# Kernel tuning notes

Hardware: AMD Instinct MI355X
Metric: run time of the kernel (lower is better)

The kernel has to match this reference:

```python
import jax, jax.numpy as jnp
from jax import lax
import numpy as np

B, C, N, T, K = 16, 64, 512, 64, 2
KSIZE, DIL = 2, 1
PAD = (KSIZE - 1) * DIL
EPS = 1e-5


def _powers(A, k):
    Ps = [jnp.eye(A.shape[0], dtype=A.dtype)]
    for _ in range(k):
        Ps.append(Ps[-1] @ A)
    return jnp.stack(Ps)  # (K+1, N, N)


def setup_inputs() -> dict:
    key = jax.random.key(0)
    ks = jax.random.split(key, 12)
    x = jax.random.normal(ks[0], (B, C, N, T), dtype=jnp.float32)
    # row-normalized random transition matrices, precomputed powers
    Af = jax.random.uniform(ks[1], (N, N), dtype=jnp.float32)
    Af = Af / Af.sum(axis=1, keepdims=True)
    Ab = Af.T / Af.T.sum(axis=1, keepdims=True)
    Aa = jax.random.uniform(ks[2], (N, N), dtype=jnp.float32)
    Aa = Aa / Aa.sum(axis=1, keepdims=True)
    P_f_pows = _powers(Af, K)
    P_b_pows = _powers(Ab, K)
    A_adp_pows = _powers(Aa, K)
    s = 0.05
    filter_w = jax.random.normal(ks[3], (C, C, 1, KSIZE), dtype=jnp.float32) * s
    filter_b = jnp.zeros((C,), jnp.float32)
    gate_w = jax.random.normal(ks[4], (C, C, 1, KSIZE), dtype=jnp.float32) * s
    gate_b = jnp.zeros((C,), jnp.float32)
    skip_w = jax.random.normal(ks[5], (C, C, 1, 1), dtype=jnp.float32) * s
    skip_b = jnp.zeros((C,), jnp.float32)
    weight_f = jax.random.normal(ks[6], (K + 1, C, C), dtype=jnp.float32) * s
    weight_b = jax.random.normal(ks[7], (K + 1, C, C), dtype=jnp.float32) * s
    gcn_bias = jnp.zeros((C,), jnp.float32)
    ln_gamma = jnp.ones((C,), jnp.float32)
    ln_beta = jnp.zeros((C,), jnp.float32)
    alpha = jnp.float32(0.5)
    return dict(x=x, P_f_pows=P_f_pows, P_b_pows=P_b_pows, A_adp_pows=A_adp_pows,
                filter_w=filter_w, filter_b=filter_b, gate_w=gate_w, gate_b=gate_b,
                skip_w=skip_w, skip_b=skip_b, weight_f=weight_f, weight_b=weight_b,
                gcn_bias=gcn_bias, ln_gamma=ln_gamma, ln_beta=ln_beta, alpha=alpha)


def _conv(x, w, b, dil=1):
    y = lax.conv_general_dilated(x, w, window_strides=(1, 1), padding='VALID',
                                 rhs_dilation=(1, dil),
                                 dimension_numbers=('NCHW', 'OIHW', 'NCHW'))
    return y + b[None, :, None, None]


def _apply_powers(xt, P_pows, weights):
    # xt: (B*T, N, Cin); P_pows: (K+1, N, N); weights: (K+1, Cin, Cout)
    xk = jnp.einsum('kij,bjc->kbic', P_pows, xt)
    return jnp.einsum('kbic,kco->bio', xk, weights)


def reference(x, P_f_pows, P_b_pows, A_adp_pows,
              filter_w, filter_b, gate_w, gate_b, skip_w, skip_b,
              weight_f, weight_b, gcn_bias, ln_gamma, ln_beta, alpha):
    # --- Gated TCN (causal left-pad along time) ---
    x_pad = jnp.pad(x, ((0, 0), (0, 0), (0, 0), (PAD, 0)))
    f = jnp.tanh(_conv(x_pad, filter_w, filter_b, DIL))
    g = jax.nn.sigmoid(_conv(x_pad, gate_w, gate_b, DIL))
    out = f * g                                   # (B, C, N, T)
    skip = _conv(out, skip_w, skip_b)             # 1x1 conv
    x_temporal = x + out                          # in_channels == out_channels

    # --- Diffusion GCN on (B*T, N, C) ---
    xt = jnp.transpose(x_temporal, (0, 3, 2, 1)).reshape(B * T, N, C)
    static_out = (_apply_powers(xt, P_f_pows, weight_f)
                  + _apply_powers(xt, P_b_pows, weight_b)
                  + gcn_bias[None, None, :])
    adapt_out = (_apply_powers(xt, A_adp_pows, weight_f)
                 + _apply_powers(xt, A_adp_pows, weight_b)
                 + gcn_bias[None, None, :])

    a = jax.nn.sigmoid(alpha)
    x_gcn = a * static_out + (1.0 - a) * adapt_out

    # --- LayerNorm over channel dim (dropout = identity in eval) ---
    mu = x_gcn.mean(axis=-1, keepdims=True)
    var = ((x_gcn - mu) ** 2).mean(axis=-1, keepdims=True)
    x_gcn = (x_gcn - mu) * lax.rsqrt(var + EPS) * ln_gamma + ln_beta

    x_out = x_gcn.reshape(B, T, N, C).transpose(0, 3, 2, 1)  # (B, C, N, T)
    return (x_out, skip)
```

## Files before the change

kernel.cpp:

```cpp
#include <hip/hip_runtime.h>
#include <cstdint>
#include <cstddef>

#define NB 16
#define NC 64
#define NN 512
#define NT 64
#define BT (NB*NT)
#define NN2 (NN*NN)
#define XSTRIDE_B (NC*NN*NT)
#define XSTRIDE_C (NN*NT)
#define XT_ROW (BT*NC)

typedef __attribute__((ext_vector_type(8))) short short8;
typedef __attribute__((ext_vector_type(4))) float f32x4;
typedef unsigned short ushort_t;
typedef unsigned int uint_t;

__device__ __forceinline__ ushort_t f2bf(float f) {
    uint_t u = __builtin_bit_cast(uint_t, f);
    u += 0x7FFFu + ((u >> 16) & 1u);
    return (ushort_t)(u >> 16);
}
__device__ __forceinline__ float bf2f(ushort_t u) {
    return __builtin_bit_cast(float, (uint_t)u << 16);
}
__device__ __forceinline__ void gl_lds16(const void* g, void* s) {
    __builtin_amdgcn_global_load_lds(
        (const __attribute__((address_space(1))) unsigned int*)g,
        (__attribute__((address_space(3))) unsigned int*)s, 16, 0, 0);
}
__device__ __forceinline__ void wait_vm(int n) {
    if (n >= 8)      asm volatile("s_waitcnt vmcnt(8)" ::: "memory");
    else if (n == 6) asm volatile("s_waitcnt vmcnt(6)" ::: "memory");
    else if (n == 4) asm volatile("s_waitcnt vmcnt(4)" ::: "memory");
    else if (n == 2) asm volatile("s_waitcnt vmcnt(2)" ::: "memory");
    else             asm volatile("s_waitcnt vmcnt(0)" ::: "memory");
}

__global__ void k_prep(const float* __restrict__ wf, const float* __restrict__ wb,
                       const float* __restrict__ alpha, ushort_t* __restrict__ Wcb) {
    int i = blockIdx.x * 256 + threadIdx.x;
    if (i >= 7 * 4096) return;
    float a = 1.f / (1.f + expf(-alpha[0]));
    int r = i >> 12, co = i & 4095;
    int c = co >> 6, o = co & 63;
    float v;
    if      (r == 0) v = wf[co] + wb[co];
    else if (r == 1) v = a * wf[4096 + co];
    else if (r == 2) v = a * wf[8192 + co];
    else if (r == 3) v = a * wb[4096 + co];
    else if (r == 4) v = a * wb[8192 + co];
    else if (r == 5) v = (1.f - a) * (wf[4096 + co] + wb[4096 + co]);
    else             v = (1.f - a) * (wf[8192 + co] + wb[8192 + co]);
    int chunk = ((c >> 5) << 2) | (o >> 4);
    int lane  = (((c >> 3) & 3) << 4) | (o & 15);
    int j     = c & 7;
    Wcb[r * 4096 + chunk * 512 + lane * 8 + j] = f2bf(v);
}

__global__ void k_prepP(const float* __restrict__ Pf, const float* __restrict__ Pb,
                        const float* __restrict__ Aa, ushort_t* __restrict__ Apk) {
    int i = blockIdx.x * 256 + threadIdx.x;
    if (i >= 196608) return;
    int lane = i & 63, kc = (i >> 6) & 15, nt = (i >> 10) & 31, r = i >> 15;
    const float* base;
    if      (r == 0) base = Pf + NN2;
    else if (r == 1) base = Pf + 2 * NN2;
    else if (r == 2) base = Pb + NN2;
    else if (r == 3) base = Pb + 2 * NN2;
    else if (r == 4) base = Aa + NN2;
    else             base = Aa + 2 * NN2;
    int n = nt * 16 + (lane & 15);
    int k0 = kc * 32 + (lane >> 4) * 8;
    const float* src = base + (size_t)n * NN + k0;
    float4 v0 = ((const float4*)src)[0];
    float4 v1 = ((const float4*)src)[1];
    uint4 o;
    o.x = (uint_t)f2bf(v0.x) | ((uint_t)f2bf(v0.y) << 16);
    o.y = (uint_t)f2bf(v0.z) | ((uint_t)f2bf(v0.w) << 16);
    o.z = (uint_t)f2bf(v1.x) | ((uint_t)f2bf(v1.y) << 16);
    o.w = (uint_t)f2bf(v1.z) | ((uint_t)f2bf(v1.w) << 16);
    *(uint4*)(Apk + (size_t)i * 8) = o;
}

__global__ void k_prepW(const float* __restrict__ fw, const float* __restrict__ gw,
                        const float* __restrict__ sw, ushort_t* __restrict__ Wt) {
    int i = blockIdx.x * 256 + threadIdx.x;
    if (i >= 5 * 4096) return;
    int mat = i >> 12, t = i & 4095;
    int chunk = t >> 9, l = (t >> 3) & 63, j = t & 7;
    int m = chunk >> 1, kb = chunk & 1;
    int o = m * 16 + (l & 15);
    int c = kb * 32 + ((l >> 4) << 3) + j;
    float v;
    if      (mat == 0) v = fw[o * 128 + c * 2 + 0];
    else if (mat == 1) v = fw[o * 128 + c * 2 + 1];
    else if (mat == 2) v = gw[o * 128 + c * 2 + 0];
    else if (mat == 3) v = gw[o * 128 + c * 2 + 1];
    else               v = sw[o * 64 + c];
    Wt[i] = f2bf(v);
}

#define XS_P 72
__device__ __forceinline__ int swzA(int r, int c) {
    return r * XS_P + (c ^ (((r >> 4) & 3) << 3));
}
__global__ __launch_bounds__(256, 3) void k_tcn(
    const float* __restrict__ x,
    const ushort_t* __restrict__ Wt,
    const float* __restrict__ fb, const float* __restrict__ gb,
    const float* __restrict__ sb,
    float* __restrict__ skip_out, ushort_t* __restrict__ XTbf) {
    __shared__ __align__(16) ushort_t Xs[65 * XS_P];
    __shared__ __align__(16) ushort_t Os[64 * XS_P];

    int tx = threadIdx.x;
    int b = blockIdx.x >> 9, n = blockIdx.x & (NN - 1);

    {
        int c = tx >> 2, tq = tx & 3, t0 = tq * 16;
        const float* src = x + (size_t)b * XSTRIDE_B + (size_t)c * XSTRIDE_C
                             + (size_t)n * NT + t0;
        float4 v0 = ((const float4*)src)[0];
        float4 v1 = ((const float4*)src)[1];
        float4 v2 = ((const float4*)src)[2];
        float4 v3 = ((const float4*)src)[3];
        float vv[16] = {v0.x, v0.y, v0.z, v0.w, v1.x, v1.y, v1.z, v1.w,
                        v2.x, v2.y, v2.z, v2.w, v3.x, v3.y, v3.z, v3.w};
#pragma unroll
        for (int e = 0; e < 16; ++e) {
            int r = t0 + e + 1;
            Xs[swzA(r, c)] = f2bf(vv[e]);
        }
        if (tx < 8) ((uint4*)Xs)[tx] = (uint4){0, 0, 0, 0};
    }
    __syncthreads();

    int w = tx >> 6, l = tx & 63, lr = l & 15, lg = l >> 4;

    short8 wf0[2], wf1[2], wg0[2], wg1[2], wsk[2];
#pragma unroll
    for (int kb = 0; kb < 2; ++kb) {
        int off = (w * 2 + kb) * 512 + l * 8;
        wf0[kb] = *(const short8*)(Wt + 0 * 4096 + off);
        wf1[kb] = *(const short8*)(Wt + 1 * 4096 + off);
        wg0[kb] = *(const short8*)(Wt + 2 * 4096 + off);
        wg1[kb] = *(const short8*)(Wt + 3 * 4096 + off);
        wsk[kb] = *(const short8*)(Wt + 4 * 4096 + off);
    }
    float fbv[4], gbv[4], sbv[4];
#pragma unroll
    for (int q = 0; q < 4; ++q) {
        int o = w * 16 + lg * 4 + q;
        fbv[q] = fb[o]; gbv[q] = gb[o]; sbv[q] = sb[o];
    }

#pragma unroll
    for (int tb = 0; tb < 4; ++tb) {
        short8 b0[2], b1[2];
#pragma unroll
        for (int kb = 0; kb < 2; ++kb) {
            int blk = kb * 4 + lg;
            int r1 = tb * 16 + lr + 1, r0 = tb * 16 + lr;
            b1[kb] = *(const short8*)&Xs[r1 * XS_P + (((blk ^ ((r1 >> 4) & 3)) << 3))];
            b0[kb] = *(const short8*)&Xs[r0 * XS_P + (((blk ^ ((r0 >> 4) & 3)) << 3))];
        }
        f32x4 aF = {fbv[0], fbv[1], fbv[2], fbv[3]};
        f32x4 aG = {gbv[0], gbv[1], gbv[2], gbv[3]};
        aF = __builtin_amdgcn_mfma_f32_16x16x32_bf16(wf0[0], b0[0], aF, 0, 0, 0);
        aF = __builtin_amdgcn_mfma_f32_16x16x32_bf16(wf0[1], b0[1], aF, 0, 0, 0);
        aF = __builtin_amdgcn_mfma_f32_16x16x32_bf16(wf1[0], b1[0], aF, 0, 0, 0);
        aF = __builtin_amdgcn_mfma_f32_16x16x32_bf16(wf1[1], b1[1], aF, 0, 0, 0);
        aG = __builtin_amdgcn_mfma_f32_16x16x32_bf16(wg0[0], b0[0], aG, 0, 0, 0);
        aG = __builtin_amdgcn_mfma_f32_16x16x32_bf16(wg0[1], b0[1], aG, 0, 0, 0);
        aG = __builtin_amdgcn_mfma_f32_16x16x32_bf16(wg1[0], b1[0], aG, 0, 0, 0);
        aG = __builtin_amdgcn_mfma_f32_16x16x32_bf16(wg1[1], b1[1], aG, 0, 0, 0);
        int t = tb * 16 + lr;
#pragma unroll
        for (int q = 0; q < 4; ++q) {
            float fo = tanhf(aF[q]);
            float go = 1.f / (1.f + expf(-aG[q]));
            int o = w * 16 + lg * 4 + q;
            Os[swzA(t, o)] = f2bf(fo * go);
        }
    }
    __syncthreads();

    float* skp = skip_out + (size_t)b * XSTRIDE_B + (size_t)n * NT;
#pragma unroll
    for (int tb = 0; tb < 4; ++tb) {
        int t = tb * 16 + lr;
        short8 ov[2];
#pragma unroll
        for (int kb = 0; kb < 2; ++kb) {
            int blk = kb * 4 + lg;
            ov[kb] = *(const short8*)&Os[t * XS_P + (((blk ^ ((t >> 4) & 3)) << 3))];
        }
        f32x4 aS = {sbv[0], sbv[1], sbv[2], sbv[3]};
        aS = __builtin_amdgcn_mfma_f32_16x16x32_bf16(wsk[0], ov[0], aS, 0, 0, 0);
        aS = __builtin_amdgcn_mfma_f32_16x16x32_bf16(wsk[1], ov[1], aS, 0, 0, 0);
#pragma unroll
        for (int q = 0; q < 4; ++q) {
            int o = w * 16 + lg * 4 + q;
            skp[(size_t)o * XSTRIDE_C + t] = aS[q];
        }
    }

    {
        int t = tx >> 2, cch = (tx & 3) * 16;
        ushort_t* dst = XTbf + (size_t)n * XT_ROW + (size_t)b * 4096 + t * 64 + cch;
        int rX = t + 1;
#pragma unroll
        for (int blk2 = 0; blk2 < 2; ++blk2) {
            int cb = (cch >> 3) + blk2;
            short8 xv = *(const short8*)&Xs[rX * XS_P + ((cb ^ ((rX >> 4) & 3)) << 3)];
            short8 ovv = *(const short8*)&Os[t * XS_P + ((cb ^ ((t >> 4) & 3)) << 3)];
            uint_t pk[4];
#pragma unroll
            for (int h = 0; h < 4; ++h) {
                float s0 = bf2f((ushort_t)xv[h * 2]) + bf2f((ushort_t)ovv[h * 2]);
                float s1 = bf2f((ushort_t)xv[h * 2 + 1]) + bf2f((ushort_t)ovv[h * 2 + 1]);
                pk[h] = (uint_t)f2bf(s0) | ((uint_t)f2bf(s1) << 16);
            }
            *(uint4*)(dst + blk2 * 8) = (uint4){pk[0], pk[1], pk[2], pk[3]};
        }
    }
}

__global__ __launch_bounds__(256) void k_tr(const ushort_t* __restrict__ XTbf,
                                            ushort_t* __restrict__ Bpk) {
    __shared__ ushort_t tile[32 * XS_P];
    int tx = threadIdx.x;
    int bt = blockIdx.x;
    int jj = tx >> 3, c8 = (tx & 7) * 8;
    int f = tx >> 6, lane = tx & 63, lg = lane >> 4, lr = lane & 15;
    for (int kc = 0; kc < 16; ++kc) {
        if (kc) __syncthreads();
        *(uint4*)&tile[jj * XS_P + c8] =
            *(const uint4*)(XTbf + (size_t)(kc * 32 + jj) * XT_ROW + bt * 64 + c8);
        __syncthreads();
        ushort_t vals[8];
#pragma unroll
        for (int e = 0; e < 8; ++e)
            vals[e] = tile[(lg * 8 + e) * XS_P + f * 16 + lr];
        uint4 o;
        o.x = (uint_t)vals[0] | ((uint_t)vals[1] << 16);
        o.y = (uint_t)vals[2] | ((uint_t)vals[3] << 16);
        o.z = (uint_t)vals[4] | ((uint_t)vals[5] << 16);
        o.w = (uint_t)vals[6] | ((uint_t)vals[7] << 16);
        *(uint4*)(Bpk + (size_t)bt * 32768 + kc * 2048 + tx * 8) = o;
    }
}

__global__ __launch_bounds__(256, 4) void k_gcn(
    const ushort_t* __restrict__ Apk,
    const ushort_t* __restrict__ Bpk,
    const ushort_t* __restrict__ XTbf,
    const ushort_t* __restrict__ Wcb,
    const float* __restrict__ bias,
    ushort_t* __restrict__ G) {
    __shared__ __align__(16) char smem[24576];

    int tx = threadIdx.x;
    int w = tx >> 6, l = tx & 63;
    int lr = l & 15, lg = l >> 4;
    int s = w >> 1, h = w & 1;

    int bid = (blockIdx.x & 7) * 2048 + (blockIdx.x >> 3);
    int bt = bid >> 4;
    int n0i = bid & 15;
    int n0 = n0i << 5;

    f32x4 acc[3][4];
#pragma unroll
    for (int j = 0; j < 3; ++j)
#pragma unroll
        for (int f = 0; f < 4; ++f) acc[j][f] = (f32x4){0.f, 0.f, 0.f, 0.f};

    const ushort_t* aBase = Apk + (size_t)(h * 3) * NN2
                                + (size_t)(n0i * 2 + s) * 8192 + l * 8;
    const ushort_t* bSrc = Bpk + (size_t)bt * 32768 + w * 512 + l * 8;

    short8 aA0[3], aA1[3], aB[3];
#pragma unroll
    for (int j = 0; j < 3; ++j) aA0[j] = *(const short8*)(aBase + (size_t)j * NN2);
#pragma unroll
    for (int d = 0; d < 4; ++d)
        gl_lds16(bSrc + d * 2048, smem + d * 4096 + w * 1024);
    wait_vm(2);
    __builtin_amdgcn_s_barrier();
    __builtin_amdgcn_sched_barrier(0);

#pragma unroll
    for (int g = 0; g < 8; ++g) {
        const int k0 = 2 * g, k1 = 2 * g + 1;
#pragma unroll
        for (int j = 0; j < 3; ++j)
            aB[j] = *(const short8*)(aBase + (size_t)j * NN2 + k1 * 512);
        if (k0 + 2 < 16) {
            if ((g & 1) == 0) {
#pragma unroll
                for (int j = 0; j < 3; ++j)
                    aA1[j] = *(const short8*)(aBase + (size_t)j * NN2 + (k0 + 2) * 512);
            } else {
#pragma unroll
                for (int j = 0; j < 3; ++j)
                    aA0[j] = *(const short8*)(aBase + (size_t)j * NN2 + (k0 + 2) * 512);
            }
        }
        if (k0 + 4 < 16)
            gl_lds16(bSrc + (k0 + 4) * 2048, smem + ((k0 + 4) % 6) * 4096 + w * 1024);
        if (k1 + 4 < 16)
            gl_lds16(bSrc + (k1 + 4) * 2048, smem + ((k1 + 4) % 6) * 4096 + w * 1024);

        {
            const char* sBr = smem + (k0 % 6) * 4096;
            short8 bv[4];
#pragma unroll
            for (int f = 0; f < 4; ++f)
                bv[f] = *(const short8*)(sBr + f * 1024 + l * 16);
            const short8 a0 = (g & 1) ? aA1[0] : aA0[0];
            const short8 a1 = (g & 1) ? aA1[1] : aA0[1];
            const short8 a2 = (g & 1) ? aA1[2] : aA0[2];
            __builtin_amdgcn_s_setprio(1);
#pragma unroll
            for (int f = 0; f < 4; ++f)
                acc[0][f] = __builtin_amdgcn_mfma_f32_16x16x32_bf16(a0, bv[f], acc[0][f], 0, 0, 0);
#pragma unroll
            for (int f = 0; f < 4; ++f)
                acc[1][f] = __builtin_amdgcn_mfma_f32_16x16x32_bf16(a1, bv[f], acc[1][f], 0, 0, 0);
#pragma unroll
            for (int f = 0; f < 4; ++f)
                acc[2][f] = __builtin_amdgcn_mfma_f32_16x16x32_bf16(a2, bv[f], acc[2][f], 0, 0, 0);
            __builtin_amdgcn_s_setprio(0);
        }
        {
            const char* sBr = smem + (k1 % 6) * 4096;
            short8 bv[4];
#pragma unroll
            for (int f = 0; f < 4; ++f)
                bv[f] = *(const short8*)(sBr + f * 1024 + l * 16);
            __builtin_amdgcn_s_setprio(1);
#pragma unroll
            for (int f = 0; f < 4; ++f)
                acc[0][f] = __builtin_amdgcn_mfma_f32_16x16x32_bf16(aB[0], bv[f], acc[0][f], 0, 0, 0);
#pragma unroll
            for (int f = 0; f < 4; ++f)
                acc[1][f] = __builtin_amdgcn_mfma_f32_16x16x32_bf16(aB[1], bv[f], acc[1][f], 0, 0, 0);
#pragma unroll
            for (int f = 0; f < 4; ++f)
                acc[2][f] = __builtin_amdgcn_mfma_f32_16x16x32_bf16(aB[2], bv[f], acc[2][f], 0, 0, 0);
            __builtin_amdgcn_s_setprio(0);
        }
        wait_vm(g <= 5 ? 8 : (g == 6 ? 6 : 0));
        __builtin_amdgcn_s_barrier();
        __builtin_amdgcn_sched_barrier(0);
    }

    float* sC = (float*)smem;
    ushort_t* sYw = (ushort_t*)(smem + 8192) + w * 1152;

    f32x4 acc2[4];
#pragma unroll
    for (int fo = 0; fo < 4; ++fo) {
        float b = (h == 0) ? bias[fo * 16 + lr] : 0.f;
        acc2[fo] = (f32x4){b, b, b, b};
    }
    const ushort_t* wBase = Wcb + l * 8;

    if (h == 0) {
        const ushort_t* xs = XTbf + (size_t)(n0 + s * 16 + lr) * XT_ROW + bt * 64 + lg * 8;
        short8 ay0 = *(const short8*)(xs);
        short8 ay1 = *(const short8*)(xs + 32);
#pragma unroll
        for (int kh = 0; kh < 2; ++kh)
#pragma unroll
            for (int fo = 0; fo < 4; ++fo) {
                short8 wv = *(const short8*)(wBase + (kh * 4 + fo) * 512);
                acc2[fo] = __builtin_amdgcn_mfma_f32_16x16x32_bf16(
                    kh ? ay1 : ay0, wv, acc2[fo], 0, 0, 0);
            }
    }
#pragma unroll
    for (int j = 0; j < 3; ++j) {
        int wcIdx = (h == 0) ? (j + 1) : (j + 4);
#pragma unroll
        for (int f = 0; f < 4; ++f)
#pragma unroll
            for (int q = 0; q < 4; ++q)
                sYw[(lg * 4 + q) * 72 + f * 16 + lr] = f2bf(acc[j][f][q]);
        short8 ay0 = *(const short8*)(&sYw[lr * 72 + lg * 8]);
        short8 ay1 = *(const short8*)(&sYw[lr * 72 + 32 + lg * 8]);
#pragma unroll
        for (int kh = 0; kh < 2; ++kh)
#pragma unroll
            for (int fo = 0; fo < 4; ++fo) {
                short8 wv = *(const short8*)(wBase + wcIdx * 4096 + (kh * 4 + fo) * 512);
                acc2[fo] = __builtin_amdgcn_mfma_f32_16x16x32_bf16(
                    kh ? ay1 : ay0, wv, acc2[fo], 0, 0, 0);
            }
    }

    if (h == 1) {
#pragma unroll
        for (int fo = 0; fo < 4; ++fo)
            *(f32x4*)&sC[(s * 4 + fo) * 256 + l * 4] = acc2[fo];
    }
    __syncthreads();
    if (h == 0) {
        ushort_t* gp = G + (size_t)(n0 + s * 16 + lg * 4) * XT_ROW + bt * 64 + lr;
#pragma unroll
        for (int fo = 0; fo < 4; ++fo) {
            f32x4 other = *(const f32x4*)&sC[(s * 4 + fo) * 256 + l * 4];
#pragma unroll
            for (int q = 0; q < 4; ++q)
                gp[(size_t)q * XT_ROW + fo * 16] = f2bf(acc2[fo][q] + other[q]);
        }
    }
}

__global__ __launch_bounds__(256) void k_ln_t(
    const ushort_t* __restrict__ G,
    const float* __restrict__ gamma, const float* __restrict__ beta,
    float* __restrict__ xout) {
    __shared__ float sT[64 * 65];
    __shared__ float sMu[64], sRs[64];
    __shared__ float sS[64 * 4], sQ[64 * 4];

    int bid = blockIdx.x;
    int b = bid >> 9, n = bid & (NN - 1);
    int tx = threadIdx.x;
    const ushort_t* src = G + (size_t)n * XT_ROW + (size_t)b * (NT * NC);

#pragma unroll
    for (int u = 0; u < 2; ++u) {
        int fi = u * 256 + tx;
        uint4 v = ((const uint4*)src)[fi];
        int t = fi >> 3, c = (fi & 7) * 8;
        sT[t * 65 + c + 0] = bf2f((ushort_t)(v.x & 0xffff));
        sT[t * 65 + c + 1] = bf2f((ushort_t)(v.x >> 16));
        sT[t * 65 + c + 2] = bf2f((ushort_t)(v.y & 0xffff));
        sT[t * 65 + c + 3] = bf2f((ushort_t)(v.y >> 16));
        sT[t * 65 + c + 4] = bf2f((ushort_t)(v.z & 0xffff));
        sT[t * 65 + c + 5] = bf2f((ushort_t)(v.z >> 16));
        sT[t * 65 + c + 6] = bf2f((ushort_t)(v.w & 0xffff));
        sT[t * 65 + c + 7] = bf2f((ushort_t)(v.w >> 16));
    }
    __syncthreads();
    {
        int row = tx >> 2, seg = tx & 3;
        float s = 0.f, q = 0.f;
        for (int cc = 0; cc < 16; ++cc) {
            float v = sT[row * 65 + seg * 16 + cc];
            s += v; q += v * v;
        }
        sS[row * 4 + seg] = s; sQ[row * 4 + seg] = q;
    }
    __syncthreads();
    if (tx < 64) {
        float ss = sS[tx * 4] + sS[tx * 4 + 1] + sS[tx * 4 + 2] + sS[tx * 4 + 3];
        float qq = sQ[tx * 4] + sQ[tx * 4 + 1] + sQ[tx * 4 + 2] + sQ[tx * 4 + 3];
        float mu = ss * (1.f / 64.f);
        float var = qq * (1.f / 64.f) - mu * mu;
        sMu[tx] = mu; sRs[tx] = rsqrtf(var + 1e-5f);
    }
    __syncthreads();
    {
        int t = tx & 63, cg = (tx >> 6) * 16;
        float mu = sMu[t], rs = sRs[t];
        for (int cc = 0; cc < 16; ++cc) {
            int c = cg + cc;
            float v = (sT[t * 65 + c] - mu) * rs * gamma[c] + beta[c];
            xout[(size_t)b * XSTRIDE_B + (size_t)c * XSTRIDE_C + (size_t)n * NT + t] = v;
        }
    }
}

extern "C" void kernel_launch(void* const* d_in, const int* in_sizes, int n_in,
                              void* d_out, int out_size, void* d_ws, size_t ws_size,
                              hipStream_t stream) {
    const float* x     = (const float*)d_in[0];
    const float* Pf    = (const float*)d_in[1];
    const float* Pb    = (const float*)d_in[2];
    const float* Aa    = (const float*)d_in[3];
    const float* fw    = (const float*)d_in[4];
    const float* fb    = (const float*)d_in[5];
    const float* gw    = (const float*)d_in[6];
    const float* gb    = (const float*)d_in[7];
    const float* sw    = (const float*)d_in[8];
    const float* sb    = (const float*)d_in[9];
    const float* wf    = (const float*)d_in[10];
    const float* wb    = (const float*)d_in[11];
    const float* gbias = (const float*)d_in[12];
    const float* lng   = (const float*)d_in[13];
    const float* lnb   = (const float*)d_in[14];
    const float* alpha = (const float*)d_in[15];

    float* xout = (float*)d_out;
    float* skip = (float*)d_out + (size_t)NB * NC * NN * NT;

    char* ws = (char*)d_ws;
    ushort_t* XTbf = (ushort_t*)(ws);
    ushort_t* Bpk  = (ushort_t*)(ws + 67108864);
    ushort_t* Gb   = (ushort_t*)(ws + 134217728);
    ushort_t* Apk  = (ushort_t*)(ws + 201326592);
    ushort_t* Wcb  = (ushort_t*)(ws + 204472320);
    ushort_t* Wt   = (ushort_t*)(ws + 204537856);

    hipLaunchKernelGGL(k_prep, dim3(112), dim3(256), 0, stream, wf, wb, alpha, Wcb);
    hipLaunchKernelGGL(k_prepW, dim3(80), dim3(256), 0, stream, fw, gw, sw, Wt);
    hipLaunchKernelGGL(k_prepP, dim3(768), dim3(256), 0, stream, Pf, Pb, Aa, Apk);
    hipLaunchKernelGGL(k_tcn, dim3(NB * NN), dim3(256), 0, stream,
                       x, Wt, fb, gb, sb, skip, XTbf);
    hipLaunchKernelGGL(k_tr, dim3(1024), dim3(256), 0, stream, XTbf, Bpk);
    hipLaunchKernelGGL(k_gcn, dim3(16384), dim3(256), 0, stream,
                       Apk, Bpk, XTbf, Wcb, gbias, Gb);
    hipLaunchKernelGGL(k_ln_t, dim3(NB * NN), dim3(256), 0, stream, Gb, lng, lnb, xout);
}
```

Measured before the change: 392.2 us.

## Restructure GCN k-loop into four-step groups with 8-slot LDS ring and fewer barriers

The main GCN MFMA loop is rewritten to process four k-steps per iteration instead of two. B tiles are prefetched into an 8-slot LDS ring (32 KB instead of 24 KB), and A fragments are register-prefetched in a rotating scheme. This halves the number of barriers and waitcnt points per tile. The larger shared memory footprint may reduce occupancy, and the wait now lets only 3 outstanding loads remain, so prefetched A register loads may be waited on earlier than before.

```diff
diff --git a/kernel.cpp b/kernel.cpp
--- a/kernel.cpp
+++ b/kernel.cpp
@@ -31,10 +31,7 @@
         (__attribute__((address_space(3))) unsigned int*)s, 16, 0, 0);
 }
 __device__ __forceinline__ void wait_vm(int n) {
-    if (n >= 8)      asm volatile("s_waitcnt vmcnt(8)" ::: "memory");
-    else if (n == 6) asm volatile("s_waitcnt vmcnt(6)" ::: "memory");
-    else if (n == 4) asm volatile("s_waitcnt vmcnt(4)" ::: "memory");
-    else if (n == 2) asm volatile("s_waitcnt vmcnt(2)" ::: "memory");
+    if (n == 3)      asm volatile("s_waitcnt vmcnt(3)" ::: "memory");
     else             asm volatile("s_waitcnt vmcnt(0)" ::: "memory");
 }
 
@@ -260,7 +257,7 @@
     const ushort_t* __restrict__ Wcb,
     const float* __restrict__ bias,
     ushort_t* __restrict__ G) {
-    __shared__ __align__(16) char smem[24576];
+    __shared__ __align__(16) char smem[32768];
 
     int tx = threadIdx.x;
     int w = tx >> 6, l = tx & 63;
@@ -282,78 +279,99 @@
                                 + (size_t)(n0i * 2 + s) * 8192 + l * 8;
     const ushort_t* bSrc = Bpk + (size_t)bt * 32768 + w * 512 + l * 8;
 
-    short8 aA0[3], aA1[3], aB[3];
-#pragma unroll
-    for (int j = 0; j < 3; ++j) aA0[j] = *(const short8*)(aBase + (size_t)j * NN2);
+    short8 aCur[3], aT1[3], aT2[3];
+#pragma unroll
+    for (int j = 0; j < 3; ++j) aCur[j] = *(const short8*)(aBase + (size_t)j * NN2);
 #pragma unroll
     for (int d = 0; d < 4; ++d)
         gl_lds16(bSrc + d * 2048, smem + d * 4096 + w * 1024);
-    wait_vm(2);
+    wait_vm(0);
     __builtin_amdgcn_s_barrier();
     __builtin_amdgcn_sched_barrier(0);
 
 #pragma unroll
-    for (int g = 0; g < 8; ++g) {
-        const int k0 = 2 * g, k1 = 2 * g + 1;
-#pragma unroll
-        for (int j = 0; j < 3; ++j)
-            aB[j] = *(const short8*)(aBase + (size_t)j * NN2 + k1 * 512);
-        if (k0 + 2 < 16) {
-            if ((g & 1) == 0) {
-#pragma unroll
-                for (int j = 0; j < 3; ++j)
-                    aA1[j] = *(const short8*)(aBase + (size_t)j * NN2 + (k0 + 2) * 512);
-            } else {
-#pragma unroll
-                for (int j = 0; j < 3; ++j)
-                    aA0[j] = *(const short8*)(aBase + (size_t)j * NN2 + (k0 + 2) * 512);
-            }
-        }
-        if (k0 + 4 < 16)
-            gl_lds16(bSrc + (k0 + 4) * 2048, smem + ((k0 + 4) % 6) * 4096 + w * 1024);
-        if (k1 + 4 < 16)
-            gl_lds16(bSrc + (k1 + 4) * 2048, smem + ((k1 + 4) % 6) * 4096 + w * 1024);
-
+    for (int g = 0; g < 4; ++g) {
+        const int k0 = 4 * g;
+#pragma unroll
+        for (int j = 0; j < 3; ++j) {
+            aT1[j] = *(const short8*)(aBase + (size_t)j * NN2 + (k0 + 1) * 512);
+            aT2[j] = *(const short8*)(aBase + (size_t)j * NN2 + (k0 + 2) * 512);
+        }
+        if (g < 3) {
+#pragma unroll
+            for (int d = 0; d < 4; ++d)
+                gl_lds16(bSrc + (k0 + 4 + d) * 2048,
+                         smem + ((k0 + 4 + d) & 7) * 4096 + w * 1024);
+        }
         {
-            const char* sBr = smem + (k0 % 6) * 4096;
-            short8 bv[4];
-#pragma unroll
-            for (int f = 0; f < 4; ++f)
-                bv[f] = *(const short8*)(sBr + f * 1024 + l * 16);
-            const short8 a0 = (g & 1) ? aA1[0] : aA0[0];
-            const short8 a1 = (g & 1) ? aA1[1] : aA0[1];
-            const short8 a2 = (g & 1) ? aA1[2] : aA0[2];
-            __builtin_amdgcn_s_setprio(1);
-#pragma unroll
-            for (int f = 0; f < 4; ++f)
-                acc[0][f] = __builtin_amdgcn_mfma_f32_16x16x32_bf16(a0, bv[f], acc[0][f], 0, 0, 0);
-#pragma unroll
-            for (int f = 0; f < 4; ++f)
-                acc[1][f] = __builtin_amdgcn_mfma_f32_16x16x32_bf16(a1, bv[f], acc[1][f], 0, 0, 0);
-#pragma unroll
-            for (int f = 0; f < 4; ++f)
-                acc[2][f] = __builtin_amdgcn_mfma_f32_16x16x32_bf16(a2, bv[f], acc[2][f], 0, 0, 0);
-            __builtin_amdgcn_s_setprio(0);
-        }
-        {
-            const char* sBr = smem + (k1 % 6) * 4096;
+            const char* sBr = smem + ((k0 + 0) & 7) * 4096;
             short8 bv[4];
 #pragma unroll
             for (int f = 0; f < 4; ++f)
                 bv[f] = *(const short8*)(sBr + f * 1024 + l * 16);
             __builtin_amdgcn_s_setprio(1);
 #pragma unroll
+            for (int j = 0; j < 3; ++j)
+#pragma unroll
+                for (int f = 0; f < 4; ++f)
+                    acc[j][f] = __builtin_amdgcn_mfma_f32_16x16x32_bf16(
+                        aCur[j], bv[f], acc[j][f], 0, 0, 0);
+            __builtin_amdgcn_s_setprio(0);
+        }
+        if (g < 3) {
+#pragma unroll
+            for (int j = 0; j < 3; ++j)
+                aCur[j] = *(const short8*)(aBase + (size_t)j * NN2 + (k0 + 4) * 512);
+        }
+        {
+            const char* sBr = smem + ((k0 + 1) & 7) * 4096;
+            short8 bv[4];
+#pragma unroll
             for (int f = 0; f < 4; ++f)
-                acc[0][f] = __builtin_amdgcn_mfma_f32_16x16x32_bf16(aB[0], bv[f], acc[0][f], 0, 0, 0);
+                bv[f] = *(const short8*)(sBr + f * 1024 + l * 16);
+            __builtin_amdgcn_s_setprio(1);
+#pragma unroll
+            for (int j = 0; j < 3; ++j)
+#pragma unroll
+                for (int f = 0; f < 4; ++f)
+                    acc[j][f] = __builtin_amdgcn_mfma_f32_16x16x32_bf16(
+                        aT1[j], bv[f], acc[j][f], 0, 0, 0);
+            __builtin_amdgcn_s_setprio(0);
+        }
+#pragma unroll
+        for (int j = 0; j < 3; ++j)
+            aT1[j] = *(const short8*)(aBase + (size_t)j * NN2 + (k0 + 3) * 512);
+        {
+            const char* sBr = smem + ((k0 + 2) & 7) * 4096;
+            short8 bv[4];
 #pragma unroll
             for (int f = 0; f < 4; ++f)
-                acc[1][f] = __builtin_amdgcn_mfma_f32_16x16x32_bf16(aB[1], bv[f], acc[1][f], 0, 0, 0);
+                bv[f] = *(const short8*)(sBr + f * 1024 + l * 16);
+            __builtin_amdgcn_s_setprio(1);
+#pragma unroll
+            for (int j = 0; j < 3; ++j)
+#pragma unroll
+                for (int f = 0; f < 4; ++f)
+                    acc[j][f] = __builtin_amdgcn_mfma_f32_16x16x32_bf16(
+                        aT2[j], bv[f], acc[j][f], 0, 0, 0);
+            __builtin_amdgcn_s_setprio(0);
+        }
+        {
+            const char* sBr = smem + ((k0 + 3) & 7) * 4096;
+            short8 bv[4];
 #pragma unroll
             for (int f = 0; f < 4; ++f)
-                acc[2][f] = __builtin_amdgcn_mfma_f32_16x16x32_bf16(aB[2], bv[f], acc[2][f], 0, 0, 0);
+                bv[f] = *(const short8*)(sBr + f * 1024 + l * 16);
+            __builtin_amdgcn_s_setprio(1);
+#pragma unroll
+            for (int j = 0; j < 3; ++j)
+#pragma unroll
+                for (int f = 0; f < 4; ++f)
+                    acc[j][f] = __builtin_amdgcn_mfma_f32_16x16x32_bf16(
+                        aT1[j], bv[f], acc[j][f], 0, 0, 0);
             __builtin_amdgcn_s_setprio(0);
         }
-        wait_vm(g <= 5 ? 8 : (g == 6 ? 6 : 0));
+        wait_vm(g < 3 ? 3 : 0);
         __builtin_amdgcn_s_barrier();
         __builtin_amdgcn_sched_barrier(0);
     }
```

New measurement: 406.4 us. 1.04x slower.
